# Kernel optimization log

Hardware: AMD Instinct MI355X
Metric: run time of the kernel (lower is better)

## Reference

```python
import jax, jax.numpy as jnp
import numpy as np

N_NODES = 100000

def gcn_conv(x, W, b, src, dst, norm, num_nodes):
    # Linear transform first (PyG GCNConv), then normalized scatter-add over edges.
    h = x @ W  # [N, d_out]
    msgs = norm[:, None] * h[src]  # gather source features, scale by sym norm
    out = jax.ops.segment_sum(msgs, dst, num_segments=num_nodes)
    return out + b

def gcn_norm(edge_index, num_nodes):
    # add self loops, compute deg^-1/2[src] * deg^-1/2[dst] per edge (PyG gcn_norm)
    loops = jnp.arange(num_nodes, dtype=edge_index.dtype)
    src = jnp.concatenate([edge_index[0], loops])
    dst = jnp.concatenate([edge_index[1], loops])
    deg = jax.ops.segment_sum(jnp.ones_like(dst, dtype=jnp.float32), dst, num_segments=num_nodes)
    dinv = jnp.where(deg > 0, jax.lax.rsqrt(deg), 0.0)
    norm = dinv[src] * dinv[dst]
    return src, dst, norm

def setup_inputs() -> dict:
    key = jax.random.key(0)
    k1, k2, k3, k4 = jax.random.split(key, 4)
    x = jax.random.normal(k1, (N_NODES, 512), dtype=jnp.float32)
    edge_index = jax.random.randint(k2, (2, 1600000), 0, N_NODES, dtype=jnp.int32)
    W1 = jax.random.normal(k3, (512, 128), dtype=jnp.float32) * (1.0 / np.sqrt(512))
    b1 = jnp.zeros((128,), dtype=jnp.float32)
    W2 = jax.random.normal(k4, (128, 40), dtype=jnp.float32) * (1.0 / np.sqrt(128))
    b2 = jnp.zeros((40,), dtype=jnp.float32)
    return {"x": x, "edge_index": edge_index, "W1": W1, "b1": b1, "W2": W2, "b2": b2}

def reference(x, edge_index, W1, b1, W2, b2):
    src, dst, norm = gcn_norm(edge_index, N_NODES)
    h = jax.nn.relu(gcn_conv(x, W1, b1, src, dst, norm, N_NODES))
    # dropout is identity in eval mode
    logits = gcn_conv(h, W2, b2, src, dst, norm, N_NODES)
    return jax.nn.log_softmax(logits, axis=1)
```

## Files before the change

kernel.cpp:

```cpp
#include <hip/hip_runtime.h>
#include <hip/hip_bf16.h>
#include <math.h>

typedef __attribute__((ext_vector_type(8))) short short8v;
typedef __attribute__((ext_vector_type(4))) unsigned short ushort4v;
typedef __attribute__((ext_vector_type(8))) unsigned short ushort8v;
typedef __attribute__((ext_vector_type(4))) unsigned uint4v;
typedef __attribute__((ext_vector_type(4))) float f32x4;

#define CAP 64

__device__ inline unsigned short f2bf(float f) {
    unsigned u = __float_as_uint(f);
    return (unsigned short)((u + 0x7fffu + ((u >> 16) & 1u)) >> 16);
}
__device__ inline float bflo(unsigned u) { return __uint_as_float(u << 16); }
__device__ inline float bfhi(unsigned u) { return __uint_as_float(u & 0xffff0000u); }
__device__ inline unsigned pk2(float a, float b) {
    __hip_bfloat162 h = __float22bfloat162_rn(make_float2(a, b));
    unsigned r;
    __builtin_memcpy(&r, &h, 4);
    return r;
}

__global__ void k_pre(const float* __restrict__ W1, unsigned short* __restrict__ Wswz,
                      const int* __restrict__ dst, int* __restrict__ deg,
                      int* __restrict__ rank, int E) {
    if (blockIdx.x < 32) {
        int t = blockIdx.x * blockDim.x + threadIdx.x;
        if (t >= 16 * 8 * 64) return;
        int l = t & 63, cb = (t >> 6) & 7, ks = t >> 9;
        int col = cb * 16 + (l & 15);
        int kb = ks * 32 + 8 * (l >> 4);
        ushort8v w;
#pragma unroll
        for (int j = 0; j < 8; ++j) w[j] = f2bf(W1[(size_t)(kb + j) * 128 + col]);
        *(ushort8v*)(Wswz + (size_t)t * 8) = w;
    } else {
        int e = (blockIdx.x - 32) * blockDim.x + threadIdx.x;
        if (e < E) rank[e] = atomicAdd(&deg[dst[e]], 1);
    }
}

#define AP 40
#define CP 132

__global__ __launch_bounds__(256) void k_fg(const float* __restrict__ x,
                                            const unsigned short* __restrict__ Wswz,
                                            const int* __restrict__ deg,
                                            unsigned short* __restrict__ h0s, int M,
                                            const int* __restrict__ esrc_in,
                                            const int* __restrict__ edst_in,
                                            const int* __restrict__ rank,
                                            int* __restrict__ esrc, int E) {
    __shared__ __align__(16) unsigned short lds[64 * CP];
    int ngemm = (M + 63) >> 6;
    if ((int)blockIdx.x >= ngemm) {
        int e = ((int)blockIdx.x - ngemm) * 256 + (int)threadIdx.x;
        if (e < E) esrc[(size_t)edst_in[e] * CAP + rank[e]] = esrc_in[e];
        return;
    }
    int tid = threadIdx.x;
    int wc = tid >> 6, lane = tid & 63;
    int g = lane >> 4, lr = lane & 15;
    int brow = blockIdx.x * 64;

    int srow = tid >> 2, sq = tid & 3;
    int sgr = brow + srow;
    const float* xp = (sgr < M) ? (x + (size_t)sgr * 512 + sq * 8) : nullptr;

    f32x4 acc[4][2];
#pragma unroll
    for (int m = 0; m < 4; ++m)
#pragma unroll
        for (int n = 0; n < 2; ++n) acc[m][n] = (f32x4){0.f, 0.f, 0.f, 0.f};

    float4 paA = make_float4(0.f, 0.f, 0.f, 0.f), pbA = paA;
    float4 paB = paA, pbB = paA;
    if (xp) {
        paA = *(const float4*)xp;          pbA = *(const float4*)(xp + 4);
        paB = *(const float4*)(xp + 32);   pbB = *(const float4*)(xp + 36);
    }

#pragma unroll 1
    for (int ks = 0; ks < 16; ks += 2) {
        {
            unsigned short* As = lds;
            union { uint4v u; short8v s; } cv;
            cv.u[0] = pk2(paA.x, paA.y); cv.u[1] = pk2(paA.z, paA.w);
            cv.u[2] = pk2(pbA.x, pbA.y); cv.u[3] = pk2(pbA.z, pbA.w);
            *(short8v*)&As[srow * AP + sq * 8] = cv.s;
            __syncthreads();
            if (ks + 2 < 16 && xp) {
                const float* np = xp + (ks + 2) * 32;
                paA = *(const float4*)np; pbA = *(const float4*)(np + 4);
            }
            short8v bfr[2];
#pragma unroll
            for (int n = 0; n < 2; ++n) {
                int cb = wc * 2 + n;
                bfr[n] = *(const short8v*)(Wswz + (size_t)((ks * 8 + cb) * 64 + lane) * 8);
            }
            short8v afr[4];
#pragma unroll
            for (int m = 0; m < 4; ++m)
                afr[m] = *(const short8v*)&As[(m * 16 + lr) * AP + g * 8];
#pragma unroll
            for (int m = 0; m < 4; ++m)
#pragma unroll
                for (int n = 0; n < 2; ++n)
                    acc[m][n] = __builtin_amdgcn_mfma_f32_16x16x32_bf16(afr[m], bfr[n],
                                                                        acc[m][n], 0, 0, 0);
        }
        {
            unsigned short* As = lds + 2560;
            union { uint4v u; short8v s; } cv;
            cv.u[0] = pk2(paB.x, paB.y); cv.u[1] = pk2(paB.z, paB.w);
            cv.u[2] = pk2(pbB.x, pbB.y); cv.u[3] = pk2(pbB.z, pbB.w);
            *(short8v*)&As[srow * AP + sq * 8] = cv.s;
            __syncthreads();
            if (ks + 3 < 16 && xp) {
                const float* np = xp + (ks + 3) * 32;
                paB = *(const float4*)np; pbB = *(const float4*)(np + 4);
            }
            int k1 = ks + 1;
            short8v bfr[2];
#pragma unroll
            for (int n = 0; n < 2; ++n) {
                int cb = wc * 2 + n;
                bfr[n] = *(const short8v*)(Wswz + (size_t)((k1 * 8 + cb) * 64 + lane) * 8);
            }
            short8v afr[4];
#pragma unroll
            for (int m = 0; m < 4; ++m)
                afr[m] = *(const short8v*)&As[(m * 16 + lr) * AP + g * 8];
#pragma unroll
            for (int m = 0; m < 4; ++m)
#pragma unroll
                for (int n = 0; n < 2; ++n)
                    acc[m][n] = __builtin_amdgcn_mfma_f32_16x16x32_bf16(afr[m], bfr[n],
                                                                        acc[m][n], 0, 0, 0);
        }
    }
    __syncthreads();
#pragma unroll
    for (int m = 0; m < 4; ++m) {
        int row0 = m * 16 + g * 4;
        float dv[4];
#pragma unroll
        for (int r = 0; r < 4; ++r) {
            int gr = brow + row0 + r;
            dv[r] = (gr < M) ? rsqrtf((float)(deg[gr] + 1)) : 0.f;
        }
#pragma unroll
        for (int n = 0; n < 2; ++n) {
            int col = wc * 32 + n * 16 + lr;
#pragma unroll
            for (int r = 0; r < 4; ++r)
                lds[(row0 + r) * CP + col] = f2bf(acc[m][n][r] * dv[r]);
        }
    }
    __syncthreads();
    if (sgr < M) {
        unsigned short* dst = h0s + (size_t)sgr * 128;
        const unsigned short* src = &lds[srow * CP];
#pragma unroll
        for (int i = 0; i < 4; ++i) {
            int c = i * 32 + sq * 8;
            *(ushort4v*)(dst + c)     = *(const ushort4v*)(src + c);
            *(ushort4v*)(dst + c + 4) = *(const ushort4v*)(src + c + 4);
        }
    }
}

__global__ __launch_bounds__(256) void k_agg1(const unsigned short* __restrict__ h0s,
                                              const int* __restrict__ deg,
                                              const int* __restrict__ esrc,
                                              const float* __restrict__ b1,
                                              unsigned* __restrict__ h1b, int N) {
    int wid = (blockIdx.x * 256 + threadIdx.x) >> 6;
    if (wid >= N) return;
    int lane = threadIdx.x & 63;
    int half = lane >> 5, hl = lane & 31;
    const uint2* base = (const uint2*)h0s;
    uint2 us = base[(size_t)wid * 32 + hl];
    float ax0, ay0, ax1, ay1;
    if (half == 0) {
        ax0 = bflo(us.x); ay0 = bfhi(us.x); ax1 = bflo(us.y); ay1 = bfhi(us.y);
    } else {
        ax0 = ay0 = ax1 = ay1 = 0.f;
    }
    int cnt = deg[wid];
    int beg = wid * CAP;
    {
        int nb = cnt;
        int idx = (lane < nb) ? esrc[beg + lane] : 0;
        int k = 0;
        for (; k + 32 <= nb; k += 32) {
            uint2 v[16];
#pragma unroll
            for (int j = 0; j < 16; ++j) {
                int s = __shfl(idx, k + 2 * j + half);
                v[j] = base[(size_t)s * 32 + hl];
            }
#pragma unroll
            for (int j = 0; j < 16; ++j) {
                ax0 += bflo(v[j].x); ay0 += bfhi(v[j].x);
                ax1 += bflo(v[j].y); ay1 += bfhi(v[j].y);
            }
        }
        for (; k + 8 <= nb; k += 8) {
            uint2 v[4];
#pragma unroll
            for (int j = 0; j < 4; ++j) {
                int s = __shfl(idx, k + 2 * j + half);
                v[j] = base[(size_t)s * 32 + hl];
            }
#pragma unroll
            for (int j = 0; j < 4; ++j) {
                ax0 += bflo(v[j].x); ay0 += bfhi(v[j].x);
                ax1 += bflo(v[j].y); ay1 += bfhi(v[j].y);
            }
        }
        for (; k + 2 <= nb; k += 2) {
            int s = __shfl(idx, k + half);
            uint2 v = base[(size_t)s * 32 + hl];
            ax0 += bflo(v.x); ay0 += bfhi(v.x);
            ax1 += bflo(v.y); ay1 += bfhi(v.y);
        }
        if (k < nb) {
            int s = __shfl(idx, k);
            uint2 v = base[(size_t)s * 32 + hl];
            if (half == 0) {
                ax0 += bflo(v.x); ay0 += bfhi(v.x);
                ax1 += bflo(v.y); ay1 += bfhi(v.y);
            }
        }
    }
    ax0 += __shfl_xor(ax0, 32); ay0 += __shfl_xor(ay0, 32);
    ax1 += __shfl_xor(ax1, 32); ay1 += __shfl_xor(ay1, 32);
    if (half == 0) {
        float di = rsqrtf((float)(cnt + 1));
        float4 bb = ((const float4*)b1)[hl];
        float r0 = fmaxf(fmaf(di, ax0, bb.x), 0.f);
        float r1 = fmaxf(fmaf(di, ay0, bb.y), 0.f);
        float r2 = fmaxf(fmaf(di, ax1, bb.z), 0.f);
        float r3 = fmaxf(fmaf(di, ay1, bb.w), 0.f);
        uint2 o;
        o.x = pk2(r0, r1);
        o.y = pk2(r2, r3);
        ((uint2*)h1b)[(size_t)wid * 32 + hl] = o;
    }
}

__global__ __launch_bounds__(256) void k_gemm2(const unsigned* __restrict__ h1b,
                                               const float* __restrict__ W2,
                                               const int* __restrict__ deg,
                                               unsigned short* __restrict__ h2s, int N) {
    __shared__ float w2s[128 * 40];
    int tid = threadIdx.x;
    for (int i = tid; i < 128 * 40; i += 256) w2s[i] = W2[i];
    __syncthreads();
    int r = blockIdx.x * 256 + tid;
    if (r >= N) return;
    const uint4v* row = (const uint4v*)(h1b + (size_t)r * 64);
    float acc[40];
#pragma unroll
    for (int c = 0; c < 40; ++c) acc[c] = 0.f;
    for (int c8 = 0; c8 < 16; ++c8) {
        uint4v u = row[c8];
        float aa[8];
#pragma unroll
        for (int j = 0; j < 4; ++j) {
            aa[2 * j]     = bflo(u[j]);
            aa[2 * j + 1] = bfhi(u[j]);
        }
        int kb = c8 * 8;
#pragma unroll
        for (int kk = 0; kk < 8; ++kk) {
            float av = aa[kk];
            const float4* wr = (const float4*)&w2s[(kb + kk) * 40];
#pragma unroll
            for (int c4 = 0; c4 < 10; ++c4) {
                float4 w = wr[c4];
                acc[c4 * 4 + 0] = fmaf(av, w.x, acc[c4 * 4 + 0]);
                acc[c4 * 4 + 1] = fmaf(av, w.y, acc[c4 * 4 + 1]);
                acc[c4 * 4 + 2] = fmaf(av, w.z, acc[c4 * 4 + 2]);
                acc[c4 * 4 + 3] = fmaf(av, w.w, acc[c4 * 4 + 3]);
            }
        }
    }
    float di = rsqrtf((float)(deg[r] + 1));
    unsigned short* op = h2s + (size_t)r * 40;
#pragma unroll
    for (int c4 = 0; c4 < 10; ++c4) {
        ushort4v w;
        w[0] = f2bf(acc[c4 * 4 + 0] * di); w[1] = f2bf(acc[c4 * 4 + 1] * di);
        w[2] = f2bf(acc[c4 * 4 + 2] * di); w[3] = f2bf(acc[c4 * 4 + 3] * di);
        *(ushort4v*)(op + c4 * 4) = w;
    }
}

__global__ __launch_bounds__(256) void k_agg2(const unsigned short* __restrict__ h2s,
                                              const int* __restrict__ deg,
                                              const int* __restrict__ esrc,
                                              const float* __restrict__ b2,
                                              float* __restrict__ out, int N) {
    int wid = (blockIdx.x * 256 + threadIdx.x) >> 6;
    if (wid >= N) return;
    int lane = threadIdx.x & 63;
    int half = lane >> 5, hl = lane & 31;
    bool act = hl < 20;
    int cc = act ? hl : 0;
    const unsigned* base = (const unsigned*)h2s;
    unsigned us = base[(size_t)wid * 20 + cc];
    float a0 = 0.f, a1 = 0.f;
    if (half == 0 && act) { a0 = bflo(us); a1 = bfhi(us); }
    int cnt = deg[wid];
    int beg = wid * CAP;
    {
        int nb = cnt;
        int idx = (lane < nb) ? esrc[beg + lane] : 0;
        int k = 0;
        for (; k + 32 <= nb; k += 32) {
            unsigned v[16];
#pragma unroll
            for (int j = 0; j < 16; ++j) {
                int s = __shfl(idx, k + 2 * j + half);
                v[j] = base[(size_t)s * 20 + cc];
            }
#pragma unroll
            for (int j = 0; j < 16; ++j) { a0 += bflo(v[j]); a1 += bfhi(v[j]); }
        }
        for (; k + 8 <= nb; k += 8) {
            unsigned v[4];
#pragma unroll
            for (int j = 0; j < 4; ++j) {
                int s = __shfl(idx, k + 2 * j + half);
                v[j] = base[(size_t)s * 20 + cc];
            }
#pragma unroll
            for (int j = 0; j < 4; ++j) { a0 += bflo(v[j]); a1 += bfhi(v[j]); }
        }
        for (; k + 2 <= nb; k += 2) {
            int s = __shfl(idx, k + half);
            unsigned v = base[(size_t)s * 20 + cc];
            a0 += bflo(v); a1 += bfhi(v);
        }
        if (k < nb) {
            int s = __shfl(idx, k);
            unsigned v = base[(size_t)s * 20 + cc];
            if (half == 0) { a0 += bflo(v); a1 += bfhi(v); }
        }
    }
    a0 += __shfl_xor(a0, 32);
    a1 += __shfl_xor(a1, 32);
    float di = rsqrtf((float)(cnt + 1));
    float lx = 0.f, ly = 0.f;
    if (act) {
        float2 bp = ((const float2*)b2)[hl];
        lx = fmaf(di, a0, bp.x);
        ly = fmaf(di, a1, bp.y);
    }
    float m = act ? fmaxf(lx, ly) : -1e30f;
#pragma unroll
    for (int o = 32; o > 0; o >>= 1) m = fmaxf(m, __shfl_xor(m, o));
    float pv = act ? (__expf(lx - m) + __expf(ly - m)) : 0.f;
    float ssum = pv;
#pragma unroll
    for (int o = 32; o > 0; o >>= 1) ssum += __shfl_xor(ssum, o);
    ssum *= 0.5f;
    if (act && half == 0) {
        float lse = __logf(ssum);
        ((float2*)out)[(size_t)wid * 20 + hl] =
            make_float2(lx - m - lse, ly - m - lse);
    }
}

extern "C" void kernel_launch(void* const* d_in, const int* in_sizes, int n_in,
                              void* d_out, int out_size, void* d_ws, size_t ws_size,
                              hipStream_t stream) {
    const float* x  = (const float*)d_in[0];
    const int*   ei = (const int*)d_in[1];
    const float* W1 = (const float*)d_in[2];
    const float* b1 = (const float*)d_in[3];
    const float* W2 = (const float*)d_in[4];
    const float* b2 = (const float*)d_in[5];
    float* out = (float*)d_out;

    int N = in_sizes[0] / 512;
    int E = in_sizes[1] / 2;
    const int* esrc_in = ei;
    const int* edst_in = ei + E;
    int ngemm = (N + 63) / 64;
    int nfill = (E + 255) / 256;

    char* p = (char*)d_ws;
    size_t off = 0;
    auto take = [&](size_t bytes) {
        size_t o = (off + 255) & ~(size_t)255;
        off = o + bytes;
        return (void*)(p + o);
    };
    unsigned short* h0s  = (unsigned short*)take((size_t)N * 128 * 2);
    unsigned*       h1b  = (unsigned*)take((size_t)N * 64 * 4);
    unsigned short* wswz = (unsigned short*)take((size_t)16 * 8 * 64 * 8 * 2);
    int*   deg  = (int*)take((size_t)N * 4);
    int*   rank = (int*)take((size_t)E * 4);
    int*   esrc = (int*)take((size_t)N * CAP * 4);
    unsigned short* h2s = h0s;

    hipMemsetAsync(deg, 0, (size_t)N * 4, stream);

    k_pre  <<<32 + nfill, 256, 0, stream>>>(W1, wswz, edst_in, deg, rank, E);
    k_fg   <<<ngemm + nfill, 256, 0, stream>>>(x, wswz, deg, h0s, N,
                                               esrc_in, edst_in, rank, esrc, E);
    k_agg1 <<<(N + 3) / 4, 256, 0, stream>>>(h0s, deg, esrc, b1, h1b, N);
    k_gemm2<<<(N + 255) / 256, 256, 0, stream>>>(h1b, W2, deg, h2s, N);
    k_agg2 <<<(N + 3) / 4, 256, 0, stream>>>(h2s, deg, esrc, b2, out, N);
}
```

Baseline: 289.0 us.

## Fuse CSR bucket fill into degree pass and widen layer-1 gather to 16B loads

The edge bucketing now writes each source index directly after the atomic rank is obtained in k_pre. This removes the intermediate rank array and the separate fill blocks that previously ran inside the GEMM kernel, saving an E-sized write and read. Separately, the layer-1 aggregation now has each quarter-wave load 16-byte rows and handle four neighbors per step instead of two, with a two-stage shuffle reduction. The cost is slightly more register use and a different tail-handling pattern.

```diff
diff --git a/kernel.cpp b/kernel.cpp
--- a/kernel.cpp
+++ b/kernel.cpp
@@ -24,8 +24,8 @@
 }
 
 __global__ void k_pre(const float* __restrict__ W1, unsigned short* __restrict__ Wswz,
-                      const int* __restrict__ dst, int* __restrict__ deg,
-                      int* __restrict__ rank, int E) {
+                      const int* __restrict__ src, const int* __restrict__ dst,
+                      int* __restrict__ deg, int* __restrict__ esrc, int E) {
     if (blockIdx.x < 32) {
         int t = blockIdx.x * blockDim.x + threadIdx.x;
         if (t >= 16 * 8 * 64) return;
@@ -38,28 +38,22 @@
         *(ushort8v*)(Wswz + (size_t)t * 8) = w;
     } else {
         int e = (blockIdx.x - 32) * blockDim.x + threadIdx.x;
-        if (e < E) rank[e] = atomicAdd(&deg[dst[e]], 1);
+        if (e < E) {
+            int d = dst[e];
+            int r = atomicAdd(&deg[d], 1);
+            esrc[(size_t)d * CAP + r] = src[e];
+        }
     }
 }
 
 #define AP 40
 #define CP 132
 
-__global__ __launch_bounds__(256) void k_fg(const float* __restrict__ x,
-                                            const unsigned short* __restrict__ Wswz,
-                                            const int* __restrict__ deg,
-                                            unsigned short* __restrict__ h0s, int M,
-                                            const int* __restrict__ esrc_in,
-                                            const int* __restrict__ edst_in,
-                                            const int* __restrict__ rank,
-                                            int* __restrict__ esrc, int E) {
+__global__ __launch_bounds__(256) void k_gemm1(const float* __restrict__ x,
+                                               const unsigned short* __restrict__ Wswz,
+                                               const int* __restrict__ deg,
+                                               unsigned short* __restrict__ h0s, int M) {
     __shared__ __align__(16) unsigned short lds[64 * CP];
-    int ngemm = (M + 63) >> 6;
-    if ((int)blockIdx.x >= ngemm) {
-        int e = ((int)blockIdx.x - ngemm) * 256 + (int)threadIdx.x;
-        if (e < E) esrc[(size_t)edst_in[e] * CAP + rank[e]] = esrc_in[e];
-        return;
-    }
     int tid = threadIdx.x;
     int wc = tid >> 6, lane = tid & 63;
     int g = lane >> 4, lr = lane & 15;
@@ -181,14 +175,18 @@
     int wid = (blockIdx.x * 256 + threadIdx.x) >> 6;
     if (wid >= N) return;
     int lane = threadIdx.x & 63;
-    int half = lane >> 5, hl = lane & 31;
-    const uint2* base = (const uint2*)h0s;
-    uint2 us = base[(size_t)wid * 32 + hl];
-    float ax0, ay0, ax1, ay1;
-    if (half == 0) {
-        ax0 = bflo(us.x); ay0 = bfhi(us.x); ax1 = bflo(us.y); ay1 = bfhi(us.y);
+    int q = lane >> 4, ql = lane & 15;
+    const uint4v* base = (const uint4v*)h0s;
+    float a[8];
+    if (q == 0) {
+        uint4v us = base[(size_t)wid * 16 + ql];
+        a[0] = bflo(us[0]); a[1] = bfhi(us[0]);
+        a[2] = bflo(us[1]); a[3] = bfhi(us[1]);
+        a[4] = bflo(us[2]); a[5] = bfhi(us[2]);
+        a[6] = bflo(us[3]); a[7] = bfhi(us[3]);
     } else {
-        ax0 = ay0 = ax1 = ay1 = 0.f;
+#pragma unroll
+        for (int i = 0; i < 8; ++i) a[i] = 0.f;
     }
     int cnt = deg[wid];
     int beg = wid * CAP;
@@ -197,59 +195,74 @@
         int idx = (lane < nb) ? esrc[beg + lane] : 0;
         int k = 0;
         for (; k + 32 <= nb; k += 32) {
-            uint2 v[16];
-#pragma unroll
-            for (int j = 0; j < 16; ++j) {
-                int s = __shfl(idx, k + 2 * j + half);
-                v[j] = base[(size_t)s * 32 + hl];
-            }
-#pragma unroll
-            for (int j = 0; j < 16; ++j) {
-                ax0 += bflo(v[j].x); ay0 += bfhi(v[j].x);
-                ax1 += bflo(v[j].y); ay1 += bfhi(v[j].y);
-            }
-        }
-        for (; k + 8 <= nb; k += 8) {
-            uint2 v[4];
+            uint4v v[8];
+#pragma unroll
+            for (int j = 0; j < 8; ++j) {
+                int s = __shfl(idx, k + 4 * j + q);
+                v[j] = base[(size_t)s * 16 + ql];
+            }
+#pragma unroll
+            for (int j = 0; j < 8; ++j) {
+                a[0] += bflo(v[j][0]); a[1] += bfhi(v[j][0]);
+                a[2] += bflo(v[j][1]); a[3] += bfhi(v[j][1]);
+                a[4] += bflo(v[j][2]); a[5] += bfhi(v[j][2]);
+                a[6] += bflo(v[j][3]); a[7] += bfhi(v[j][3]);
+            }
+        }
+        for (; k + 16 <= nb; k += 16) {
+            uint4v v[4];
 #pragma unroll
             for (int j = 0; j < 4; ++j) {
-                int s = __shfl(idx, k + 2 * j + half);
-                v[j] = base[(size_t)s * 32 + hl];
+                int s = __shfl(idx, k + 4 * j + q);
+                v[j] = base[(size_t)s * 16 + ql];
             }
 #pragma unroll
             for (int j = 0; j < 4; ++j) {
-                ax0 += bflo(v[j].x); ay0 += bfhi(v[j].x);
-                ax1 += bflo(v[j].y); ay1 += bfhi(v[j].y);
-            }
-        }
-        for (; k + 2 <= nb; k += 2) {
-            int s = __shfl(idx, k + half);
-            uint2 v = base[(size_t)s * 32 + hl];
-            ax0 += bflo(v.x); ay0 += bfhi(v.x);
-            ax1 += bflo(v.y); ay1 += bfhi(v.y);
-        }
-        if (k < nb) {
-            int s = __shfl(idx, k);
-            uint2 v = base[(size_t)s * 32 + hl];
-            if (half == 0) {
-                ax0 += bflo(v.x); ay0 += bfhi(v.x);
-                ax1 += bflo(v.y); ay1 += bfhi(v.y);
-            }
-        }
-    }
-    ax0 += __shfl_xor(ax0, 32); ay0 += __shfl_xor(ay0, 32);
-    ax1 += __shfl_xor(ax1, 32); ay1 += __shfl_xor(ay1, 32);
-    if (half == 0) {
+                a[0] += bflo(v[j][0]); a[1] += bfhi(v[j][0]);
+                a[2] += bflo(v[j][1]); a[3] += bfhi(v[j][1]);
+                a[4] += bflo(v[j][2]); a[5] += bfhi(v[j][2]);
+                a[6] += bflo(v[j][3]); a[7] += bfhi(v[j][3]);
+            }
+        }
+        for (; k + 4 <= nb; k += 4) {
+            int s = __shfl(idx, k + q);
+            uint4v v = base[(size_t)s * 16 + ql];
+            a[0] += bflo(v[0]); a[1] += bfhi(v[0]);
+            a[2] += bflo(v[1]); a[3] += bfhi(v[1]);
+            a[4] += bflo(v[2]); a[5] += bfhi(v[2]);
+            a[6] += bflo(v[3]); a[7] += bfhi(v[3]);
+        }
+        int r = nb - k;
+        if (q < r) {
+            int s = __shfl(idx, k + q);
+            uint4v v = base[(size_t)s * 16 + ql];
+            a[0] += bflo(v[0]); a[1] += bfhi(v[0]);
+            a[2] += bflo(v[1]); a[3] += bfhi(v[1]);
+            a[4] += bflo(v[2]); a[5] += bfhi(v[2]);
+            a[6] += bflo(v[3]); a[7] += bfhi(v[3]);
+        }
+    }
+#pragma unroll
+    for (int i = 0; i < 8; ++i) {
+        a[i] += __shfl_xor(a[i], 16);
+        a[i] += __shfl_xor(a[i], 32);
+    }
+    if (q == 0) {
         float di = rsqrtf((float)(cnt + 1));
-        float4 bb = ((const float4*)b1)[hl];
-        float r0 = fmaxf(fmaf(di, ax0, bb.x), 0.f);
-        float r1 = fmaxf(fmaf(di, ay0, bb.y), 0.f);
-        float r2 = fmaxf(fmaf(di, ax1, bb.z), 0.f);
-        float r3 = fmaxf(fmaf(di, ay1, bb.w), 0.f);
-        uint2 o;
-        o.x = pk2(r0, r1);
-        o.y = pk2(r2, r3);
-        ((uint2*)h1b)[(size_t)wid * 32 + hl] = o;
+        float4 bb0 = ((const float4*)b1)[ql * 2];
+        float4 bb1 = ((const float4*)b1)[ql * 2 + 1];
+        float r0 = fmaxf(fmaf(di, a[0], bb0.x), 0.f);
+        float r1 = fmaxf(fmaf(di, a[1], bb0.y), 0.f);
+        float r2 = fmaxf(fmaf(di, a[2], bb0.z), 0.f);
+        float r3 = fmaxf(fmaf(di, a[3], bb0.w), 0.f);
+        float r4 = fmaxf(fmaf(di, a[4], bb1.x), 0.f);
+        float r5 = fmaxf(fmaf(di, a[5], bb1.y), 0.f);
+        float r6 = fmaxf(fmaf(di, a[6], bb1.z), 0.f);
+        float r7 = fmaxf(fmaf(di, a[7], bb1.w), 0.f);
+        uint4v o;
+        o[0] = pk2(r0, r1); o[1] = pk2(r2, r3);
+        o[2] = pk2(r4, r5); o[3] = pk2(r6, r7);
+        ((uint4v*)h1b)[(size_t)wid * 16 + ql] = o;
     }
 }
 
@@ -406,15 +419,13 @@
     unsigned*       h1b  = (unsigned*)take((size_t)N * 64 * 4);
     unsigned short* wswz = (unsigned short*)take((size_t)16 * 8 * 64 * 8 * 2);
     int*   deg  = (int*)take((size_t)N * 4);
-    int*   rank = (int*)take((size_t)E * 4);
     int*   esrc = (int*)take((size_t)N * CAP * 4);
     unsigned short* h2s = h0s;
 
     hipMemsetAsync(deg, 0, (size_t)N * 4, stream);
 
-    k_pre  <<<32 + nfill, 256, 0, stream>>>(W1, wswz, edst_in, deg, rank, E);
-    k_fg   <<<ngemm + nfill, 256, 0, stream>>>(x, wswz, deg, h0s, N,
-                                               esrc_in, edst_in, rank, esrc, E);
+    k_pre  <<<32 + nfill, 256, 0, stream>>>(W1, wswz, esrc_in, edst_in, deg, esrc, E);
+    k_gemm1<<<ngemm, 256, 0, stream>>>(x, wswz, deg, h0s, N);
     k_agg1 <<<(N + 3) / 4, 256, 0, stream>>>(h0s, deg, esrc, b1, h1b, N);
     k_gemm2<<<(N + 255) / 256, 256, 0, stream>>>(h1b, W2, deg, h2s, N);
     k_agg2 <<<(N + 3) / 4, 256, 0, stream>>>(h2s, deg, esrc, b2, out, N);
```

Measured after the change: 329.9 us. 1.14x slower.
